# Kernel tuning notes

Hardware: AMD Instinct MI355X
Metric: run time of the kernel (lower is better)

Reference implementation:

```python
import jax, jax.numpy as jnp
import numpy as np


def _ssm_layer(x, A, B, C, bias):
    # x: [Bt, T, D]; diagonal linear recurrence s_t = sigmoid(A)*s_{t-1} + B*x_t; y_t = C*s_t + bias
    a = jax.nn.sigmoid(A)

    def step(s, xt):
        s = a * s + B * xt
        return s, C * s + bias

    xT = jnp.swapaxes(x, 0, 1)  # [T, Bt, D]
    s0 = jnp.zeros(x.shape[::2], dtype=x.dtype)  # [Bt, D]
    _, yT = jax.lax.scan(step, s0, xT)
    return jnp.swapaxes(yT, 0, 1)  # [Bt, T, D]


def setup_inputs() -> dict:
    key = jax.random.key(0)
    ks = jax.random.split(key, 6)
    Bt, T, F, H, L = 8, 4096, 512, 1024, 4
    x = jax.random.normal(ks[0], (Bt, T, F), dtype=jnp.float32)
    W_in = jax.random.normal(ks[1], (F, H), dtype=jnp.float32) * (1.0 / np.sqrt(F))
    b_in = jnp.zeros((H,), dtype=jnp.float32)
    A = jax.random.uniform(ks[2], (L, H), dtype=jnp.float32)  # torch.rand init
    B = jax.random.normal(ks[3], (L, H), dtype=jnp.float32)
    C = jax.random.normal(ks[4], (L, H), dtype=jnp.float32)
    bias = jnp.zeros((L, H), dtype=jnp.float32)
    return {"x": x, "W_in": W_in, "b_in": b_in, "A": A, "B": B, "C": C, "bias": bias}


def reference(x, W_in, b_in, A, B, C, bias):
    # in_proj (dropout is identity at p=0)
    y = jnp.einsum('btf,fh->bth', x, W_in) + b_in
    n_layers = A.shape[0]
    for l in range(n_layers):  # small fixed layer count
        y = _ssm_layer(y, A[l], B[l], C[l], bias[l])
    # return_sequence=True, unidirectional -> y: [B, T, H]
    return y
```

## Files before the change

kernel.cpp:

```cpp
#include <hip/hip_runtime.h>
#include <hip/hip_bf16.h>
#include <stdint.h>

#define BT     8
#define T_SEQ  4096
#define K_F    512
#define N_H    1024
#define M_TOT  (BT * T_SEQ)
#define NLAYER 4
#define LC     32
#define NC     (T_SEQ / LC)

typedef short  bf16x8 __attribute__((ext_vector_type(8)));
typedef float  f32x4  __attribute__((ext_vector_type(4)));
typedef ushort u16x8  __attribute__((ext_vector_type(8)));
typedef ushort u16x4  __attribute__((ext_vector_type(4)));

__device__ __forceinline__ ushort f2bf(float f) {
  uint32_t u = __builtin_bit_cast(uint32_t, f);
  u += 0x7fffu + ((u >> 16) & 1u);
  return (ushort)(u >> 16);
}
__device__ __forceinline__ float bf2f(ushort u) {
  uint32_t x = (uint32_t)u << 16;
  return __builtin_bit_cast(float, x);
}

__device__ __forceinline__ void gload16(const void* g, void* l) {
  __builtin_amdgcn_global_load_lds(
      (const __attribute__((address_space(1))) uint32_t*)g,
      (__attribute__((address_space(3))) uint32_t*)l, 16, 0, 0);
}

#define CVT_BLOCKS ((M_TOT * K_F) / (256 * 8))

__global__ __launch_bounds__(256) void prep_kernel(const float* __restrict__ x,
                                                   ushort* __restrict__ xb,
                                                   const float* __restrict__ W,
                                                   ushort* __restrict__ Wt) {
  __shared__ float tile[32][33];
  const int bid = blockIdx.x;
  if (bid < CVT_BLOCKS) {
    const int i = bid * 256 + threadIdx.x;
    const float4* xv = (const float4*)x;
    float4 v0 = xv[2 * i + 0];
    float4 v1 = xv[2 * i + 1];
    u16x8 o;
    o[0] = f2bf(v0.x); o[1] = f2bf(v0.y); o[2] = f2bf(v0.z); o[3] = f2bf(v0.w);
    o[4] = f2bf(v1.x); o[5] = f2bf(v1.y); o[6] = f2bf(v1.z); o[7] = f2bf(v1.w);
    *((u16x8*)xb + i) = o;
  } else {
    const int idx = bid - CVT_BLOCKS;
    const int k0 = (idx & 15) * 32;
    const int n0 = (idx >> 4) * 32;
    const int lx = threadIdx.x & 31;
    const int ly = threadIdx.x >> 5;
#pragma unroll
    for (int j = 0; j < 32; j += 8)
      tile[ly + j][lx] = W[(size_t)(k0 + ly + j) * N_H + n0 + lx];
    __syncthreads();
#pragma unroll
    for (int j = 0; j < 32; j += 8)
      Wt[(size_t)(n0 + ly + j) * K_F + k0 + lx] = f2bf(tile[lx][ly + j]);
  }
}

#define BM 128
#define BN 128
#define BKK 64

__global__ __launch_bounds__(256) void gemm_kernel(
    const ushort* __restrict__ Xb, const ushort* __restrict__ Wt,
    const float* __restrict__ bias, ushort* __restrict__ Yb,
    const float* __restrict__ As, const float* __restrict__ Bs,
    const float* __restrict__ Cs, const float* __restrict__ Ds,
    float* __restrict__ E) {
  __shared__ ushort lds[BM * BKK * 2];
  ushort* lsA = lds;
  ushort* lsB = lds + BM * BKK;
  const int tid  = threadIdx.x;
  const int lane = tid & 63;
  const int wv   = tid >> 6;
  const int wr   = wv >> 1;
  const int wc   = wv & 1;
  const int m0   = blockIdx.x * BM;
  const int n0   = blockIdx.y * BN;

  const int srow = (lane >> 3);
  const int scol = (lane & 7) * 8;
  const ushort* gA = Xb + (size_t)m0 * K_F + scol;
  const ushort* gB = Wt + (size_t)n0 * K_F + scol;

  f32x4 acc[4][4];
#pragma unroll
  for (int i = 0; i < 4; i++)
#pragma unroll
    for (int j = 0; j < 4; j++) acc[i][j] = (f32x4)0.0f;

  const int lr = lane & 15;
  const int kg = (lane >> 4) * 8;

  for (int kt = 0; kt < K_F; kt += BKK) {
#pragma unroll
    for (int i = 0; i < 4; i++) {
      const int reg = wv * 4 + i;
      const int r   = reg * 8 + srow;
      gload16(gA + (size_t)r * K_F + kt, &lsA[reg * 512]);
      gload16(gB + (size_t)r * K_F + kt, &lsB[reg * 512]);
    }
    __syncthreads();

    bf16x8 af[4][2], bfr[4][2];
#pragma unroll
    for (int fm = 0; fm < 4; fm++)
#pragma unroll
      for (int kk = 0; kk < 2; kk++)
        af[fm][kk] = *(const bf16x8*)&lsA[(wr * 64 + fm * 16 + lr) * BKK + kk * 32 + kg];
#pragma unroll
    for (int fn = 0; fn < 4; fn++)
#pragma unroll
      for (int kk = 0; kk < 2; kk++)
        bfr[fn][kk] = *(const bf16x8*)&lsB[(wc * 64 + fn * 16 + lr) * BKK + kk * 32 + kg];

#pragma unroll
    for (int kk = 0; kk < 2; kk++)
#pragma unroll
      for (int fm = 0; fm < 4; fm++)
#pragma unroll
        for (int fn = 0; fn < 4; fn++)
          acc[fm][fn] = __builtin_amdgcn_mfma_f32_16x16x32_bf16(af[fm][kk], bfr[fn][kk],
                                                                acc[fm][fn], 0, 0, 0);
    __syncthreads();
  }

#pragma unroll
  for (int fn = 0; fn < 4; fn++) {
    const int col = wc * 64 + fn * 16 + lr;
    const float bv = bias[n0 + col];
#pragma unroll
    for (int fm = 0; fm < 4; fm++) {
      const int row0 = wr * 64 + fm * 16 + (lane >> 4) * 4;
#pragma unroll
      for (int i = 0; i < 4; i++)
        lds[(row0 + i) * BN + col] = f2bf(acc[fm][fn][i] + bv);
    }
  }
  __syncthreads();

  const int erow = tid >> 4;
  const int ecol = (tid & 15) * 8;
#pragma unroll
  for (int p = 0; p < 8; p++) {
    const int row = p * 16 + erow;
    u16x8 v = *(const u16x8*)&lds[row * BN + ecol];
    *(u16x8*)&Yb[(size_t)(m0 + row) * N_H + n0 + ecol] = v;
  }

  {
    const int bidx = m0 >> 12;
    const int c0   = (m0 & (T_SEQ - 1)) >> 5;
    const int hl   = tid & 127;
    const int ck0  = tid >> 7;
    const int h    = n0 + hl;

    float a[4], bb[4], cc[4], dd[4];
#pragma unroll
    for (int l = 0; l < 4; l++) {
      a[l]  = 1.f / (1.f + __expf(-As[l * N_H + h]));
      bb[l] = Bs[l * N_H + h];
      cc[l] = Cs[l * N_H + h];
      dd[l] = Ds[l * N_H + h];
    }

#pragma unroll
    for (int p = 0; p < 2; p++) {
      const int ck = ck0 + p * 2;
      float s[4] = {0.f, 0.f, 0.f, 0.f};
#pragma unroll 4
      for (int t = 0; t < LC; t++) {
        float xv = bf2f(lds[(ck * LC + t) * BN + hl]);
#pragma unroll
        for (int l = 0; l < 4; l++) {
          s[l] = fmaf(a[l], s[l], bb[l] * xv);
          xv = fmaf(cc[l], s[l], dd[l]);
        }
      }
      f32x4 e;
      e[0] = s[0]; e[1] = s[1]; e[2] = s[2]; e[3] = s[3];
      ((f32x4*)E)[(size_t)(bidx * NC + c0 + ck) * N_H + h] = e;
    }
  }
}

__global__ __launch_bounds__(256) void chunk_scan_kernel(
    const float* __restrict__ A, const float* __restrict__ B,
    const float* __restrict__ C, const float* __restrict__ E,
    float* __restrict__ S) {
  const int idx = blockIdx.x * 256 + threadIdx.x;
  const int b = idx >> 10;
  const int h = idx & (N_H - 1);

  float a[4], bcoef[4], ccoef[4];
#pragma unroll
  for (int l = 0; l < 4; l++) {
    a[l] = 1.f / (1.f + __expf(-A[l * N_H + h]));
    bcoef[l] = B[l * N_H + h];
    ccoef[l] = C[l * N_H + h];
  }

  float m[4][4] = {};
  m[0][0] = a[0];
  m[1][0] = bcoef[1] * ccoef[0] * a[0];
  m[1][1] = a[1];
  m[2][0] = bcoef[2] * ccoef[1] * m[1][0];
  m[2][1] = bcoef[2] * ccoef[1] * a[1];
  m[2][2] = a[2];
  m[3][0] = bcoef[3] * ccoef[2] * m[2][0];
  m[3][1] = bcoef[3] * ccoef[2] * m[2][1];
  m[3][2] = bcoef[3] * ccoef[2] * a[2];
  m[3][3] = a[3];

#pragma unroll
  for (int it = 0; it < 5; it++) {
    float t[4][4];
#pragma unroll
    for (int i = 0; i < 4; i++)
#pragma unroll
      for (int j = 0; j < 4; j++) {
        float acc = 0.f;
#pragma unroll
        for (int k = 0; k < 4; k++) acc = fmaf(m[i][k], m[k][j], acc);
        t[i][j] = acc;
      }
#pragma unroll
    for (int i = 0; i < 4; i++)
#pragma unroll
      for (int j = 0; j < 4; j++) m[i][j] = t[i][j];
  }

  float s[4] = {0.f, 0.f, 0.f, 0.f};
  const f32x4* Ep = (const f32x4*)E + (size_t)b * NC * N_H + h;
  f32x4* Sp = (f32x4*)S + (size_t)b * NC * N_H + h;
#pragma unroll 4
  for (int c = 0; c < NC; c++) {
    f32x4 sv;
    sv[0] = s[0]; sv[1] = s[1]; sv[2] = s[2]; sv[3] = s[3];
    Sp[(size_t)c * N_H] = sv;
    f32x4 e = Ep[(size_t)c * N_H];
    float ns[4];
#pragma unroll
    for (int i = 0; i < 4; i++) {
      float acc = e[i];
#pragma unroll
      for (int k = 0; k < 4; k++) acc = fmaf(m[i][k], s[k], acc);
      ns[i] = acc;
    }
#pragma unroll
    for (int i = 0; i < 4; i++) s[i] = ns[i];
  }
}

__global__ __launch_bounds__(256) void chunk_apply_kernel(
    const ushort* __restrict__ Yb, float* __restrict__ out,
    const float* __restrict__ A, const float* __restrict__ B,
    const float* __restrict__ C, const float* __restrict__ D,
    const float* __restrict__ S) {
  const int b  = blockIdx.x / NC;
  const int c  = blockIdx.x % NC;
  const int h4 = threadIdx.x << 2;

  float a[4][4], bb[4][4], cc[4][4], dd[4][4];
#pragma unroll
  for (int l = 0; l < 4; l++) {
    f32x4 av = *(const f32x4*)(A + l * N_H + h4);
    f32x4 bv = *(const f32x4*)(B + l * N_H + h4);
    f32x4 cv = *(const f32x4*)(C + l * N_H + h4);
    f32x4 dv = *(const f32x4*)(D + l * N_H + h4);
#pragma unroll
    for (int ch = 0; ch < 4; ch++) {
      a[l][ch]  = 1.f / (1.f + __expf(-av[ch]));
      bb[l][ch] = bv[ch]; cc[l][ch] = cv[ch]; dd[l][ch] = dv[ch];
    }
  }

  float s[4][4];
  const f32x4* sp = (const f32x4*)S + (size_t)(b * NC + c) * N_H + h4;
#pragma unroll
  for (int ch = 0; ch < 4; ch++) {
    f32x4 sv = sp[ch];
    s[0][ch] = sv[0]; s[1][ch] = sv[1]; s[2][ch] = sv[2]; s[3][ch] = sv[3];
  }

  const ushort* ybase = Yb + ((size_t)b * T_SEQ + (size_t)c * LC) * N_H + h4;
  f32x4* op = (f32x4*)(out + ((size_t)b * T_SEQ + (size_t)c * LC) * N_H) + (h4 >> 2);
#pragma unroll 4
  for (int t = 0; t < LC; t++) {
    u16x4 xv = *(const u16x4*)(ybase + (size_t)t * N_H);
    f32x4 ov;
#pragma unroll
    for (int ch = 0; ch < 4; ch++) {
      float x = bf2f(xv[ch]);
#pragma unroll
      for (int l = 0; l < 4; l++) {
        s[l][ch] = fmaf(a[l][ch], s[l][ch], bb[l][ch] * x);
        x = fmaf(cc[l][ch], s[l][ch], dd[l][ch]);
      }
      ov[ch] = x;
    }
    op[(size_t)t * (N_H / 4)] = ov;
  }
}

extern "C" void kernel_launch(void* const* d_in, const int* in_sizes, int n_in,
                              void* d_out, int out_size, void* d_ws, size_t ws_size,
                              hipStream_t stream) {
  const float* x    = (const float*)d_in[0];
  const float* W    = (const float*)d_in[1];
  const float* b_in = (const float*)d_in[2];
  const float* A    = (const float*)d_in[3];
  const float* B    = (const float*)d_in[4];
  const float* C    = (const float*)d_in[5];
  const float* bias = (const float*)d_in[6];
  float* out = (float*)d_out;

  char* wsb = (char*)d_ws;
  ushort* xb = (ushort*)wsb;
  ushort* Wt = (ushort*)(wsb + (size_t)33 * 1024 * 1024 - (size_t)N_H * K_F * 2);
  ushort* Yb = (ushort*)(wsb + (size_t)40 * 1024 * 1024);
  float*  E  = (float*)(wsb + (size_t)112 * 1024 * 1024);
  float*  S  = E + (size_t)BT * NC * N_H * 4;

  prep_kernel<<<CVT_BLOCKS + 512, 256, 0, stream>>>(x, xb, W, Wt);
  gemm_kernel<<<dim3(M_TOT / BM, N_H / BN), 256, 0, stream>>>(xb, Wt, b_in, Yb,
                                                              A, B, C, bias, E);
  chunk_scan_kernel<<<(BT * N_H) / 256, 256, 0, stream>>>(A, B, C, E, S);
  chunk_apply_kernel<<<BT * NC, 256, 0, stream>>>(Yb, out, A, B, C, bias, S);
}
```

Before: 157.3 us.

## Fuse x fp32-to-bf16 conversion into GEMM with full-K resident A tile

Result: slower. 165.1 us (+5.0%).

```diff
diff --git a/kernel.cpp b/kernel.cpp
--- a/kernel.cpp
+++ b/kernel.cpp
@@ -32,162 +32,171 @@
       (__attribute__((address_space(3))) uint32_t*)l, 16, 0, 0);
 }
 
-#define CVT_BLOCKS ((M_TOT * K_F) / (256 * 8))
-
-__global__ __launch_bounds__(256) void prep_kernel(const float* __restrict__ x,
-                                                   ushort* __restrict__ xb,
-                                                   const float* __restrict__ W,
-                                                   ushort* __restrict__ Wt) {
+__global__ __launch_bounds__(256) void prep_w_kernel(const float* __restrict__ W,
+                                                     ushort* __restrict__ Wt) {
   __shared__ float tile[32][33];
-  const int bid = blockIdx.x;
-  if (bid < CVT_BLOCKS) {
-    const int i = bid * 256 + threadIdx.x;
-    const float4* xv = (const float4*)x;
-    float4 v0 = xv[2 * i + 0];
-    float4 v1 = xv[2 * i + 1];
-    u16x8 o;
-    o[0] = f2bf(v0.x); o[1] = f2bf(v0.y); o[2] = f2bf(v0.z); o[3] = f2bf(v0.w);
-    o[4] = f2bf(v1.x); o[5] = f2bf(v1.y); o[6] = f2bf(v1.z); o[7] = f2bf(v1.w);
-    *((u16x8*)xb + i) = o;
-  } else {
-    const int idx = bid - CVT_BLOCKS;
-    const int k0 = (idx & 15) * 32;
-    const int n0 = (idx >> 4) * 32;
-    const int lx = threadIdx.x & 31;
-    const int ly = threadIdx.x >> 5;
-#pragma unroll
-    for (int j = 0; j < 32; j += 8)
-      tile[ly + j][lx] = W[(size_t)(k0 + ly + j) * N_H + n0 + lx];
-    __syncthreads();
-#pragma unroll
-    for (int j = 0; j < 32; j += 8)
-      Wt[(size_t)(n0 + ly + j) * K_F + k0 + lx] = f2bf(tile[lx][ly + j]);
-  }
-}
-
-#define BM 128
-#define BN 128
-#define BKK 64
-
-__global__ __launch_bounds__(256) void gemm_kernel(
-    const ushort* __restrict__ Xb, const ushort* __restrict__ Wt,
+  const int k0 = (blockIdx.x & 15) * 32;
+  const int n0 = (blockIdx.x >> 4) * 32;
+  const int lx = threadIdx.x & 31;
+  const int ly = threadIdx.x >> 5;
+#pragma unroll
+  for (int j = 0; j < 32; j += 8)
+    tile[ly + j][lx] = W[(size_t)(k0 + ly + j) * N_H + n0 + lx];
+  __syncthreads();
+#pragma unroll
+  for (int j = 0; j < 32; j += 8)
+    Wt[(size_t)(n0 + ly + j) * K_F + k0 + lx] = f2bf(tile[lx][ly + j]);
+}
+
+__global__ __launch_bounds__(512) void gemm_fused(
+    const float* __restrict__ x, const ushort* __restrict__ Wt,
     const float* __restrict__ bias, ushort* __restrict__ Yb,
     const float* __restrict__ As, const float* __restrict__ Bs,
     const float* __restrict__ Cs, const float* __restrict__ Ds,
     float* __restrict__ E) {
-  __shared__ ushort lds[BM * BKK * 2];
-  ushort* lsA = lds;
-  ushort* lsB = lds + BM * BKK;
+  __shared__ ushort lsA[128 * 512];
+  __shared__ ushort lsB[2][128 * 64];
+  ushort* tile = &lsB[0][0];
+
   const int tid  = threadIdx.x;
   const int lane = tid & 63;
   const int wv   = tid >> 6;
-  const int wr   = wv >> 1;
-  const int wc   = wv & 1;
-  const int m0   = blockIdx.x * BM;
-  const int n0   = blockIdx.y * BN;
-
-  const int srow = (lane >> 3);
-  const int scol = (lane & 7) * 8;
-  const ushort* gA = Xb + (size_t)m0 * K_F + scol;
-  const ushort* gB = Wt + (size_t)n0 * K_F + scol;
-
-  f32x4 acc[4][4];
-#pragma unroll
-  for (int i = 0; i < 4; i++)
-#pragma unroll
-    for (int j = 0; j < 4; j++) acc[i][j] = (f32x4)0.0f;
-
-  const int lr = lane & 15;
-  const int kg = (lane >> 4) * 8;
-
-  for (int kt = 0; kt < K_F; kt += BKK) {
-#pragma unroll
-    for (int i = 0; i < 4; i++) {
-      const int reg = wv * 4 + i;
-      const int r   = reg * 8 + srow;
-      gload16(gA + (size_t)r * K_F + kt, &lsA[reg * 512]);
-      gload16(gB + (size_t)r * K_F + kt, &lsB[reg * 512]);
+  const int wr   = wv >> 2;
+  const int wc   = wv & 3;
+  const int m0   = blockIdx.x * 128;
+  const int lr   = lane & 15;
+  const int kg   = (lane >> 4) * 8;
+  const int aswz = (lane & 7) << 3;
+
+  {
+    const float4* xs = (const float4*)(x + (size_t)m0 * K_F);
+#pragma unroll
+    for (int j = 0; j < 32; j++) {
+      const int e4  = j * 512 + tid;
+      float4 v = xs[e4];
+      const int row = e4 >> 7;
+      const int ek4 = (e4 & 127) * 4;
+      u16x4 o;
+      o[0] = f2bf(v.x); o[1] = f2bf(v.y); o[2] = f2bf(v.z); o[3] = f2bf(v.w);
+      *(u16x4*)&lsA[row * 512 + (ek4 ^ ((row & 7) << 3))] = o;
+    }
+#pragma unroll
+    for (int i = 0; i < 2; i++) {
+      const int reg = wv * 2 + i;
+      gload16(Wt + (size_t)(reg * 8 + (lane >> 3)) * K_F + (lane & 7) * 8,
+              &lsB[0][reg * 512]);
+    }
+  }
+  __syncthreads();
+
+  for (int nt = 0; nt < 8; nt++) {
+    const int n0 = nt * 128;
+    const ushort* WtN = Wt + (size_t)n0 * K_F + (lane & 7) * 8;
+
+    f32x4 acc[4][2];
+#pragma unroll
+    for (int fm = 0; fm < 4; fm++)
+#pragma unroll
+      for (int fn = 0; fn < 2; fn++) acc[fm][fn] = (f32x4)0.0f;
+
+#pragma unroll
+    for (int kt = 0; kt < 8; kt++) {
+      if (kt < 7) {
+#pragma unroll
+        for (int i = 0; i < 2; i++) {
+          const int reg = wv * 2 + i;
+          gload16(WtN + (size_t)(reg * 8 + (lane >> 3)) * K_F + (kt + 1) * 64,
+                  &lsB[(kt + 1) & 1][reg * 512]);
+        }
+      }
+
+      const ushort* lb = &lsB[kt & 1][0];
+      bf16x8 af[4][2], bfr[2][2];
+#pragma unroll
+      for (int fn = 0; fn < 2; fn++)
+#pragma unroll
+        for (int kk = 0; kk < 2; kk++)
+          bfr[fn][kk] = *(const bf16x8*)&lb[(wc * 32 + fn * 16 + lr) * 64 + kk * 32 + kg];
+#pragma unroll
+      for (int fm = 0; fm < 4; fm++) {
+        const int row = wr * 64 + fm * 16 + lr;
+#pragma unroll
+        for (int kk = 0; kk < 2; kk++)
+          af[fm][kk] = *(const bf16x8*)&lsA[row * 512 + ((kt * 64 + kk * 32 + kg) ^ aswz)];
+      }
+#pragma unroll
+      for (int kk = 0; kk < 2; kk++)
+#pragma unroll
+        for (int fm = 0; fm < 4; fm++)
+#pragma unroll
+          for (int fn = 0; fn < 2; fn++)
+            acc[fm][fn] = __builtin_amdgcn_mfma_f32_16x16x32_bf16(af[fm][kk], bfr[fn][kk],
+                                                                  acc[fm][fn], 0, 0, 0);
+      __syncthreads();
+    }
+
+#pragma unroll
+    for (int fn = 0; fn < 2; fn++) {
+      const int col = wc * 32 + fn * 16 + lr;
+      const float bv = bias[n0 + col];
+#pragma unroll
+      for (int fm = 0; fm < 4; fm++) {
+        const int row0 = wr * 64 + fm * 16 + (lane >> 4) * 4;
+#pragma unroll
+        for (int i = 0; i < 4; i++)
+          tile[(row0 + i) * 128 + col] = f2bf(acc[fm][fn][i] + bv);
+      }
     }
     __syncthreads();
 
-    bf16x8 af[4][2], bfr[4][2];
-#pragma unroll
-    for (int fm = 0; fm < 4; fm++)
-#pragma unroll
-      for (int kk = 0; kk < 2; kk++)
-        af[fm][kk] = *(const bf16x8*)&lsA[(wr * 64 + fm * 16 + lr) * BKK + kk * 32 + kg];
-#pragma unroll
-    for (int fn = 0; fn < 4; fn++)
-#pragma unroll
-      for (int kk = 0; kk < 2; kk++)
-        bfr[fn][kk] = *(const bf16x8*)&lsB[(wc * 64 + fn * 16 + lr) * BKK + kk * 32 + kg];
-
-#pragma unroll
-    for (int kk = 0; kk < 2; kk++)
-#pragma unroll
-      for (int fm = 0; fm < 4; fm++)
-#pragma unroll
-        for (int fn = 0; fn < 4; fn++)
-          acc[fm][fn] = __builtin_amdgcn_mfma_f32_16x16x32_bf16(af[fm][kk], bfr[fn][kk],
-                                                                acc[fm][fn], 0, 0, 0);
-    __syncthreads();
-  }
-
-#pragma unroll
-  for (int fn = 0; fn < 4; fn++) {
-    const int col = wc * 64 + fn * 16 + lr;
-    const float bv = bias[n0 + col];
-#pragma unroll
-    for (int fm = 0; fm < 4; fm++) {
-      const int row0 = wr * 64 + fm * 16 + (lane >> 4) * 4;
-#pragma unroll
-      for (int i = 0; i < 4; i++)
-        lds[(row0 + i) * BN + col] = f2bf(acc[fm][fn][i] + bv);
-    }
-  }
-  __syncthreads();
-
-  const int erow = tid >> 4;
-  const int ecol = (tid & 15) * 8;
-#pragma unroll
-  for (int p = 0; p < 8; p++) {
-    const int row = p * 16 + erow;
-    u16x8 v = *(const u16x8*)&lds[row * BN + ecol];
-    *(u16x8*)&Yb[(size_t)(m0 + row) * N_H + n0 + ecol] = v;
-  }
-
-  {
-    const int bidx = m0 >> 12;
-    const int c0   = (m0 & (T_SEQ - 1)) >> 5;
-    const int hl   = tid & 127;
-    const int ck0  = tid >> 7;
-    const int h    = n0 + hl;
-
-    float a[4], bb[4], cc[4], dd[4];
-#pragma unroll
-    for (int l = 0; l < 4; l++) {
-      a[l]  = 1.f / (1.f + __expf(-As[l * N_H + h]));
-      bb[l] = Bs[l * N_H + h];
-      cc[l] = Cs[l * N_H + h];
-      dd[l] = Ds[l * N_H + h];
-    }
-
-#pragma unroll
-    for (int p = 0; p < 2; p++) {
-      const int ck = ck0 + p * 2;
+    {
+      const int erow = tid >> 4;
+      const int ecol = (tid & 15) * 8;
+#pragma unroll
+      for (int p = 0; p < 4; p++) {
+        const int row = p * 32 + erow;
+        *(u16x8*)&Yb[(size_t)(m0 + row) * N_H + n0 + ecol] =
+            *(const u16x8*)&tile[row * 128 + ecol];
+      }
+    }
+    {
+      const int ck = tid >> 7;
+      const int hl = tid & 127;
+      const int h  = n0 + hl;
+      float a[4], bb[4], cc[4], dd[4];
+#pragma unroll
+      for (int l = 0; l < 4; l++) {
+        a[l]  = 1.f / (1.f + __expf(-As[l * N_H + h]));
+        bb[l] = Bs[l * N_H + h];
+        cc[l] = Cs[l * N_H + h];
+        dd[l] = Ds[l * N_H + h];
+      }
       float s[4] = {0.f, 0.f, 0.f, 0.f};
 #pragma unroll 4
       for (int t = 0; t < LC; t++) {
-        float xv = bf2f(lds[(ck * LC + t) * BN + hl]);
+        float xv = bf2f(tile[(ck * LC + t) * 128 + hl]);
 #pragma unroll
         for (int l = 0; l < 4; l++) {
           s[l] = fmaf(a[l], s[l], bb[l] * xv);
           xv = fmaf(cc[l], s[l], dd[l]);
         }
       }
+      const int bidx = m0 >> 12;
+      const int c0   = (m0 & (T_SEQ - 1)) >> 5;
       f32x4 e;
       e[0] = s[0]; e[1] = s[1]; e[2] = s[2]; e[3] = s[3];
       ((f32x4*)E)[(size_t)(bidx * NC + c0 + ck) * N_H + h] = e;
+    }
+    __syncthreads();
+
+    if (nt < 7) {
+#pragma unroll
+      for (int i = 0; i < 2; i++) {
+        const int reg = wv * 2 + i;
+        gload16(Wt + (size_t)((nt + 1) * 128 + reg * 8 + (lane >> 3)) * K_F + (lane & 7) * 8,
+                &lsB[0][reg * 512]);
+      }
+      __syncthreads();
     }
   }
 }
@@ -324,15 +333,13 @@
   float* out = (float*)d_out;
 
   char* wsb = (char*)d_ws;
-  ushort* xb = (ushort*)wsb;
-  ushort* Wt = (ushort*)(wsb + (size_t)33 * 1024 * 1024 - (size_t)N_H * K_F * 2);
-  ushort* Yb = (ushort*)(wsb + (size_t)40 * 1024 * 1024);
+  ushort* Wt = (ushort*)wsb;
+  ushort* Yb = (ushort*)(wsb + (size_t)8 * 1024 * 1024);
   float*  E  = (float*)(wsb + (size_t)112 * 1024 * 1024);
   float*  S  = E + (size_t)BT * NC * N_H * 4;
 
-  prep_kernel<<<CVT_BLOCKS + 512, 256, 0, stream>>>(x, xb, W, Wt);
-  gemm_kernel<<<dim3(M_TOT / BM, N_H / BN), 256, 0, stream>>>(xb, Wt, b_in, Yb,
-                                                              A, B, C, bias, E);
+  prep_w_kernel<<<512, 256, 0, stream>>>(W, Wt);
+  gemm_fused<<<M_TOT / 128, 512, 0, stream>>>(x, Wt, b_in, Yb, A, B, C, bias, E);
   chunk_scan_kernel<<<(BT * N_H) / 256, 256, 0, stream>>>(A, B, C, E, S);
   chunk_apply_kernel<<<BT * NC, 256, 0, stream>>>(Yb, out, A, B, C, bias, S);
 }
```

## Enlarge GEMM M tile to 256 rows with 512 threads and split epilogue

Applied to the files above, without the earlier changes.

New measurement: 173.7 us. 1.1x slower.

```diff
diff --git a/kernel.cpp b/kernel.cpp
--- a/kernel.cpp
+++ b/kernel.cpp
@@ -65,19 +65,21 @@
   }
 }
 
-#define BM 128
+#define BM 256
 #define BN 128
 #define BKK 64
 
-__global__ __launch_bounds__(256) void gemm_kernel(
+__global__ __launch_bounds__(512) void gemm_kernel(
     const ushort* __restrict__ Xb, const ushort* __restrict__ Wt,
     const float* __restrict__ bias, ushort* __restrict__ Yb,
     const float* __restrict__ As, const float* __restrict__ Bs,
     const float* __restrict__ Cs, const float* __restrict__ Ds,
     float* __restrict__ E) {
-  __shared__ ushort lds[BM * BKK * 2];
-  ushort* lsA = lds;
-  ushort* lsB = lds + BM * BKK;
+  __shared__ ushort lds[24576];
+  ushort* lsA  = lds;
+  ushort* lsB  = lds + 16384;
+  ushort* tile = lds;
+
   const int tid  = threadIdx.x;
   const int lane = tid & 63;
   const int wv   = tid >> 6;
@@ -104,9 +106,12 @@
 #pragma unroll
     for (int i = 0; i < 4; i++) {
       const int reg = wv * 4 + i;
-      const int r   = reg * 8 + srow;
-      gload16(gA + (size_t)r * K_F + kt, &lsA[reg * 512]);
-      gload16(gB + (size_t)r * K_F + kt, &lsB[reg * 512]);
+      gload16(gA + (size_t)(reg * 8 + srow) * K_F + kt, &lsA[reg * 512]);
+    }
+#pragma unroll
+    for (int i = 0; i < 2; i++) {
+      const int reg = wv * 2 + i;
+      gload16(gB + (size_t)(reg * 8 + srow) * K_F + kt, &lsB[reg * 512]);
     }
     __syncthreads();
 
@@ -133,62 +138,65 @@
     __syncthreads();
   }
 
-#pragma unroll
-  for (int fn = 0; fn < 4; fn++) {
-    const int col = wc * 64 + fn * 16 + lr;
-    const float bv = bias[n0 + col];
-#pragma unroll
-    for (int fm = 0; fm < 4; fm++) {
-      const int row0 = wr * 64 + fm * 16 + (lane >> 4) * 4;
-#pragma unroll
-      for (int i = 0; i < 4; i++)
-        lds[(row0 + i) * BN + col] = f2bf(acc[fm][fn][i] + bv);
-    }
-  }
-  __syncthreads();
-
-  const int erow = tid >> 4;
-  const int ecol = (tid & 15) * 8;
-#pragma unroll
-  for (int p = 0; p < 8; p++) {
-    const int row = p * 16 + erow;
-    u16x8 v = *(const u16x8*)&lds[row * BN + ecol];
-    *(u16x8*)&Yb[(size_t)(m0 + row) * N_H + n0 + ecol] = v;
-  }
-
-  {
-    const int bidx = m0 >> 12;
-    const int c0   = (m0 & (T_SEQ - 1)) >> 5;
-    const int hl   = tid & 127;
-    const int ck0  = tid >> 7;
-    const int h    = n0 + hl;
-
-    float a[4], bb[4], cc[4], dd[4];
-#pragma unroll
-    for (int l = 0; l < 4; l++) {
-      a[l]  = 1.f / (1.f + __expf(-As[l * N_H + h]));
-      bb[l] = Bs[l * N_H + h];
-      cc[l] = Cs[l * N_H + h];
-      dd[l] = Ds[l * N_H + h];
-    }
-
-#pragma unroll
-    for (int p = 0; p < 2; p++) {
-      const int ck = ck0 + p * 2;
+  const int bidx = m0 >> 12;
+  const int c0   = (m0 & (T_SEQ - 1)) >> 5;
+
+  const int hl = tid & 127;
+  const int h  = n0 + hl;
+  float ca[4], cb[4], cc[4], cd[4];
+#pragma unroll
+  for (int l = 0; l < 4; l++) {
+    ca[l] = 1.f / (1.f + __expf(-As[l * N_H + h]));
+    cb[l] = Bs[l * N_H + h];
+    cc[l] = Cs[l * N_H + h];
+    cd[l] = Ds[l * N_H + h];
+  }
+
+#pragma unroll
+  for (int half = 0; half < 2; half++) {
+    if ((wr >> 1) == half) {
+#pragma unroll
+      for (int fn = 0; fn < 4; fn++) {
+        const int col = wc * 64 + fn * 16 + lr;
+        const float bv = bias[n0 + col];
+#pragma unroll
+        for (int fm = 0; fm < 4; fm++) {
+          const int row0 = (wr & 1) * 64 + fm * 16 + (lane >> 4) * 4;
+#pragma unroll
+          for (int i = 0; i < 4; i++)
+            tile[(row0 + i) * BN + col] = f2bf(acc[fm][fn][i] + bv);
+        }
+      }
+    }
+    __syncthreads();
+
+    {
+      const int erow = tid >> 4;
+      const int ecol = (tid & 15) * 8;
+#pragma unroll
+      for (int p = 0; p < 4; p++) {
+        const int row = p * 32 + erow;
+        *(u16x8*)&Yb[(size_t)(m0 + half * 128 + row) * N_H + n0 + ecol] =
+            *(const u16x8*)&tile[row * BN + ecol];
+      }
+    }
+    {
+      const int ck = tid >> 7;
       float s[4] = {0.f, 0.f, 0.f, 0.f};
 #pragma unroll 4
       for (int t = 0; t < LC; t++) {
-        float xv = bf2f(lds[(ck * LC + t) * BN + hl]);
+        float xv = bf2f(tile[(ck * LC + t) * BN + hl]);
 #pragma unroll
         for (int l = 0; l < 4; l++) {
-          s[l] = fmaf(a[l], s[l], bb[l] * xv);
-          xv = fmaf(cc[l], s[l], dd[l]);
+          s[l] = fmaf(ca[l], s[l], cb[l] * xv);
+          xv = fmaf(cc[l], s[l], cd[l]);
         }
       }
       f32x4 e;
       e[0] = s[0]; e[1] = s[1]; e[2] = s[2]; e[3] = s[3];
-      ((f32x4*)E)[(size_t)(bidx * NC + c0 + ck) * N_H + h] = e;
-    }
+      ((f32x4*)E)[(size_t)(bidx * NC + c0 + half * 4 + ck) * N_H + h] = e;
+    }
+    __syncthreads();
   }
 }
 
@@ -331,7 +339,7 @@
   float*  S  = E + (size_t)BT * NC * N_H * 4;
 
   prep_kernel<<<CVT_BLOCKS + 512, 256, 0, stream>>>(x, xb, W, Wt);
-  gemm_kernel<<<dim3(M_TOT / BM, N_H / BN), 256, 0, stream>>>(xb, Wt, b_in, Yb,
+  gemm_kernel<<<dim3(M_TOT / BM, N_H / BN), 512, 0, stream>>>(xb, Wt, b_in, Yb,
                                                               A, B, C, bias, E);
   chunk_scan_kernel<<<(BT * N_H) / 256, 256, 0, stream>>>(A, B, C, E, S);
   chunk_apply_kernel<<<BT * NC, 256, 0, stream>>>(Yb, out, A, B, C, bias, S);
```

## Fuse fp32-to-bf16 conversion of x into GEMM A-tile loading

Applied to the files above, without the earlier changes.

Result: slower. 165.0 us (+4.9%).

```diff
diff --git a/kernel.cpp b/kernel.cpp
--- a/kernel.cpp
+++ b/kernel.cpp
@@ -25,6 +25,11 @@
   uint32_t x = (uint32_t)u << 16;
   return __builtin_bit_cast(float, x);
 }
+__device__ __forceinline__ uint32_t cvtpk(float lo, float hi) {
+  uint32_t r;
+  asm("v_cvt_pk_bf16_f32 %0, %1, %2" : "=v"(r) : "v"(lo), "v"(hi));
+  return r;
+}
 
 __device__ __forceinline__ void gload16(const void* g, void* l) {
   __builtin_amdgcn_global_load_lds(
@@ -32,45 +37,30 @@
       (__attribute__((address_space(3))) uint32_t*)l, 16, 0, 0);
 }
 
-#define CVT_BLOCKS ((M_TOT * K_F) / (256 * 8))
-
-__global__ __launch_bounds__(256) void prep_kernel(const float* __restrict__ x,
-                                                   ushort* __restrict__ xb,
-                                                   const float* __restrict__ W,
-                                                   ushort* __restrict__ Wt) {
+__global__ __launch_bounds__(256) void prep_w_kernel(const float* __restrict__ W,
+                                                     ushort* __restrict__ Wt) {
   __shared__ float tile[32][33];
-  const int bid = blockIdx.x;
-  if (bid < CVT_BLOCKS) {
-    const int i = bid * 256 + threadIdx.x;
-    const float4* xv = (const float4*)x;
-    float4 v0 = xv[2 * i + 0];
-    float4 v1 = xv[2 * i + 1];
-    u16x8 o;
-    o[0] = f2bf(v0.x); o[1] = f2bf(v0.y); o[2] = f2bf(v0.z); o[3] = f2bf(v0.w);
-    o[4] = f2bf(v1.x); o[5] = f2bf(v1.y); o[6] = f2bf(v1.z); o[7] = f2bf(v1.w);
-    *((u16x8*)xb + i) = o;
-  } else {
-    const int idx = bid - CVT_BLOCKS;
-    const int k0 = (idx & 15) * 32;
-    const int n0 = (idx >> 4) * 32;
-    const int lx = threadIdx.x & 31;
-    const int ly = threadIdx.x >> 5;
-#pragma unroll
-    for (int j = 0; j < 32; j += 8)
-      tile[ly + j][lx] = W[(size_t)(k0 + ly + j) * N_H + n0 + lx];
-    __syncthreads();
-#pragma unroll
-    for (int j = 0; j < 32; j += 8)
-      Wt[(size_t)(n0 + ly + j) * K_F + k0 + lx] = f2bf(tile[lx][ly + j]);
-  }
+  const int k0 = (blockIdx.x & 15) * 32;
+  const int n0 = (blockIdx.x >> 4) * 32;
+  const int lx = threadIdx.x & 31;
+  const int ly = threadIdx.x >> 5;
+#pragma unroll
+  for (int j = 0; j < 32; j += 8)
+    tile[ly + j][lx] = W[(size_t)(k0 + ly + j) * N_H + n0 + lx];
+  __syncthreads();
+#pragma unroll
+  for (int j = 0; j < 32; j += 8)
+    Wt[(size_t)(n0 + ly + j) * K_F + k0 + lx] = f2bf(tile[lx][ly + j]);
 }
 
 #define BM 128
 #define BN 128
 #define BKK 64
 
+__global__ __launch_bounds__(512) void dummy_unused();
+
 __global__ __launch_bounds__(256) void gemm_kernel(
-    const ushort* __restrict__ Xb, const ushort* __restrict__ Wt,
+    const float* __restrict__ x, const ushort* __restrict__ Wt,
     const float* __restrict__ bias, ushort* __restrict__ Yb,
     const float* __restrict__ As, const float* __restrict__ Bs,
     const float* __restrict__ Cs, const float* __restrict__ Ds,
@@ -78,6 +68,8 @@
   __shared__ ushort lds[BM * BKK * 2];
   ushort* lsA = lds;
   ushort* lsB = lds + BM * BKK;
+  ushort* tile = lds;
+
   const int tid  = threadIdx.x;
   const int lane = tid & 63;
   const int wv   = tid >> 6;
@@ -86,9 +78,18 @@
   const int m0   = blockIdx.x * BM;
   const int n0   = blockIdx.y * BN;
 
+  const int lr = lane & 15;
+  const int kg = (lane >> 4) * 8;
+  const int aswz = (lr & 7) << 3;
+
+  const int arow_lo = tid >> 4;
+  const int acol4   = tid & 15;
+  const int wswz    = (arow_lo & 7) << 3;
+  const int adst    = (acol4 * 4) ^ wswz;
+  const float4* xs  = (const float4*)(x + (size_t)m0 * K_F);
+
   const int srow = (lane >> 3);
   const int scol = (lane & 7) * 8;
-  const ushort* gA = Xb + (size_t)m0 * K_F + scol;
   const ushort* gB = Wt + (size_t)n0 * K_F + scol;
 
   f32x4 acc[4][4];
@@ -97,25 +98,37 @@
 #pragma unroll
     for (int j = 0; j < 4; j++) acc[i][j] = (f32x4)0.0f;
 
-  const int lr = lane & 15;
-  const int kg = (lane >> 4) * 8;
-
-  for (int kt = 0; kt < K_F; kt += BKK) {
+  for (int kt8 = 0; kt8 < 8; kt8++) {
+    float4 av[8];
+#pragma unroll
+    for (int j = 0; j < 8; j++)
+      av[j] = xs[(size_t)(j * 16 + arow_lo) * (K_F / 4) + kt8 * 16 + acol4];
+
+    __syncthreads();
+
+#pragma unroll
+    for (int j = 0; j < 8; j++) {
+      uint2 r;
+      r.x = cvtpk(av[j].x, av[j].y);
+      r.y = cvtpk(av[j].z, av[j].w);
+      *(uint2*)&lsA[(j * 16 + arow_lo) * BKK + adst] = r;
+    }
 #pragma unroll
     for (int i = 0; i < 4; i++) {
       const int reg = wv * 4 + i;
-      const int r   = reg * 8 + srow;
-      gload16(gA + (size_t)r * K_F + kt, &lsA[reg * 512]);
-      gload16(gB + (size_t)r * K_F + kt, &lsB[reg * 512]);
-    }
+      gload16(gB + (size_t)(reg * 8 + srow) * K_F + kt8 * 64, &lsB[reg * 512]);
+    }
+
     __syncthreads();
 
     bf16x8 af[4][2], bfr[4][2];
 #pragma unroll
-    for (int fm = 0; fm < 4; fm++)
+    for (int fm = 0; fm < 4; fm++) {
+      const int row = wr * 64 + fm * 16 + lr;
 #pragma unroll
       for (int kk = 0; kk < 2; kk++)
-        af[fm][kk] = *(const bf16x8*)&lsA[(wr * 64 + fm * 16 + lr) * BKK + kk * 32 + kg];
+        af[fm][kk] = *(const bf16x8*)&lsA[row * BKK + ((kk * 32 + kg) ^ aswz)];
+    }
 #pragma unroll
     for (int fn = 0; fn < 4; fn++)
 #pragma unroll
@@ -130,8 +143,8 @@
         for (int fn = 0; fn < 4; fn++)
           acc[fm][fn] = __builtin_amdgcn_mfma_f32_16x16x32_bf16(af[fm][kk], bfr[fn][kk],
                                                                 acc[fm][fn], 0, 0, 0);
-    __syncthreads();
-  }
+  }
+  __syncthreads();
 
 #pragma unroll
   for (int fn = 0; fn < 4; fn++) {
@@ -142,20 +155,21 @@
       const int row0 = wr * 64 + fm * 16 + (lane >> 4) * 4;
 #pragma unroll
       for (int i = 0; i < 4; i++)
-        lds[(row0 + i) * BN + col] = f2bf(acc[fm][fn][i] + bv);
+        tile[(row0 + i) * BN + col] = f2bf(acc[fm][fn][i] + bv);
     }
   }
   __syncthreads();
 
-  const int erow = tid >> 4;
-  const int ecol = (tid & 15) * 8;
-#pragma unroll
-  for (int p = 0; p < 8; p++) {
-    const int row = p * 16 + erow;
-    u16x8 v = *(const u16x8*)&lds[row * BN + ecol];
-    *(u16x8*)&Yb[(size_t)(m0 + row) * N_H + n0 + ecol] = v;
-  }
-
+  {
+    const int erow = tid >> 4;
+    const int ecol = (tid & 15) * 8;
+#pragma unroll
+    for (int p = 0; p < 8; p++) {
+      const int row = p * 16 + erow;
+      *(u16x8*)&Yb[(size_t)(m0 + row) * N_H + n0 + ecol] =
+          *(const u16x8*)&tile[row * BN + ecol];
+    }
+  }
   {
     const int bidx = m0 >> 12;
     const int c0   = (m0 & (T_SEQ - 1)) >> 5;
@@ -171,14 +185,13 @@
       cc[l] = Cs[l * N_H + h];
       dd[l] = Ds[l * N_H + h];
     }
-
 #pragma unroll
     for (int p = 0; p < 2; p++) {
       const int ck = ck0 + p * 2;
       float s[4] = {0.f, 0.f, 0.f, 0.f};
 #pragma unroll 4
       for (int t = 0; t < LC; t++) {
-        float xv = bf2f(lds[(ck * LC + t) * BN + hl]);
+        float xv = bf2f(tile[(ck * LC + t) * BN + hl]);
 #pragma unroll
         for (int l = 0; l < 4; l++) {
           s[l] = fmaf(a[l], s[l], bb[l] * xv);
@@ -324,14 +337,13 @@
   float* out = (float*)d_out;
 
   char* wsb = (char*)d_ws;
-  ushort* xb = (ushort*)wsb;
-  ushort* Wt = (ushort*)(wsb + (size_t)33 * 1024 * 1024 - (size_t)N_H * K_F * 2);
-  ushort* Yb = (ushort*)(wsb + (size_t)40 * 1024 * 1024);
+  ushort* Wt = (ushort*)wsb;
+  ushort* Yb = (ushort*)(wsb + (size_t)8 * 1024 * 1024);
   float*  E  = (float*)(wsb + (size_t)112 * 1024 * 1024);
   float*  S  = E + (size_t)BT * NC * N_H * 4;
 
-  prep_kernel<<<CVT_BLOCKS + 512, 256, 0, stream>>>(x, xb, W, Wt);
-  gemm_kernel<<<dim3(M_TOT / BM, N_H / BN), 256, 0, stream>>>(xb, Wt, b_in, Yb,
+  prep_w_kernel<<<512, 256, 0, stream>>>(W, Wt);
+  gemm_kernel<<<dim3(M_TOT / BM, N_H / BN), 256, 0, stream>>>(x, Wt, b_in, Yb,
                                                               A, B, C, bias, E);
   chunk_scan_kernel<<<(BT * N_H) / 256, 256, 0, stream>>>(A, B, C, E, S);
   chunk_apply_kernel<<<BT * NC, 256, 0, stream>>>(Yb, out, A, B, C, bias, S);
```
